# Kernel optimization log

Measured on AMD Instinct MI355X. Metric: run time of the kernel, lower is better.

The kernel has to match this reference:

```python
import jax, jax.numpy as jnp
import numpy as np
import math

N = 6144
HID = 128
HEADS = 4
DEG = 32


def setup_inputs() -> dict:
    key = jax.random.key(0)
    ks = jax.random.split(key, 8)
    H = jax.random.normal(ks[0], (N, HID), dtype=jnp.float32)
    # random edges + self-loops so every row has at least one valid entry
    src = jax.random.randint(ks[1], (N * DEG,), 0, N)
    dst = jax.random.randint(ks[2], (N * DEG,), 0, N)
    loops = jnp.arange(N)
    edge_index = jnp.stack([jnp.concatenate([src, loops]),
                            jnp.concatenate([dst, loops])], axis=0).astype(jnp.int64)
    s = 1.0 / math.sqrt(HID)
    Wq = jax.random.normal(ks[3], (HID, HID * HEADS), dtype=jnp.float32) * s
    Wk = jax.random.normal(ks[4], (HID, HID * HEADS), dtype=jnp.float32) * s
    Wv = jax.random.normal(ks[5], (HID, HID * HEADS), dtype=jnp.float32) * s
    Wp = jax.random.normal(ks[6], (HID * HEADS, HID), dtype=jnp.float32) * (1.0 / math.sqrt(HID * HEADS))
    bp = jnp.zeros((HID,), dtype=jnp.float32)
    return {"H": H, "edge_index": edge_index, "Wq": Wq, "Wk": Wk, "Wv": Wv, "Wp": Wp, "bp": bp}


def reference(H, edge_index, Wq, Wk, Wv, Wp, bp):
    n = H.shape[0]
    q = (H @ Wq).reshape(n, HEADS, HID)
    k = (H @ Wk).reshape(n, HEADS, HID)
    v = (H @ Wv).reshape(n, HEADS, HID)
    # dense boolean edge mask [N, N]
    mask = jnp.zeros((n, n), dtype=bool).at[edge_index[0], edge_index[1]].set(True)
    scores = jnp.einsum('nhd,mhd->hnm', q, k) / math.sqrt(HID)
    scores = jnp.where(mask[None, :, :], scores, -jnp.inf)
    alpha = jax.nn.softmax(scores, axis=-1)
    out = jnp.einsum('hnm,mhd->nhd', alpha, v).reshape(n, HEADS * HID)
    return out @ Wp + bp
```

## Files before the change

### kernel.cpp

```cpp
#include <hip/hip_runtime.h>
#include <hip/hip_bf16.h>


#define N_NODES 6144
#define HIDC 128
#define QKV_N 1536
#define OUT_N 512
#define MASK_WPR 192

typedef __bf16 bf16;
typedef __attribute__((ext_vector_type(8))) __bf16 bf16x8;
typedef __attribute__((ext_vector_type(4))) float f32x4;

__global__ void k_detect_f(const unsigned* __restrict__ Hw, int* __restrict__ fflag) {
    int lane = threadIdx.x;
    unsigned w = Hw[lane];
    int el = (w >> 7) & 0xFF;
    unsigned long long b = __ballot(el >= 110 && el <= 135);
    if (lane == 0) *fflag = (__popcll(b) >= 32) ? 0 : 1;
}

__global__ void k_detect_e(const int* __restrict__ e32, int* __restrict__ eflag) {
    int lane = threadIdx.x;
    unsigned long long b = __ballot(e32[2 * lane + 1] == 0);
    if (lane == 0) *eflag = (b == ~0ull) ? 1 : 0;
}

__global__ __launch_bounds__(256) void k_build_mask(const int* __restrict__ e32, int E,
                                                    const int* __restrict__ eflag,
                                                    unsigned* __restrict__ mask) {
    int e = blockIdx.x * blockDim.x + threadIdx.x;
    if (e >= E) return;
    int s, d;
    if (*eflag) { s = e32[2 * e];  d = e32[2 * E + 2 * e]; }
    else        { s = e32[e];      d = e32[E + e]; }
    if ((unsigned)s < N_NODES && (unsigned)d < N_NODES)
        atomicOr(&mask[s * MASK_WPR + (d >> 5)], 1u << (d & 31));
}

__global__ __launch_bounds__(256) void k_cast_all(const void* __restrict__ H,
                                                  const void* __restrict__ Wq,
                                                  const void* __restrict__ Wk,
                                                  const void* __restrict__ Wv,
                                                  const void* __restrict__ Wp,
                                                  bf16* __restrict__ Hc,
                                                  bf16* __restrict__ Wt_qkv,
                                                  bf16* __restrict__ Wpt,
                                                  const int* __restrict__ fflag) {
    int b = blockIdx.x;
    int t = threadIdx.x;
    int f = *fflag;
    if (b < 3072) {
        int i = b * 256 + t;
        Hc[i] = f ? (bf16)((const float*)H)[i] : ((const bf16*)H)[i];
    } else if (b < 3840) {
        int s = (b - 3072) >> 8;
        int e = ((b - 3072) & 255) * 256 + t;
        int n = e >> 7, k = e & 127;
        const void* W = (s == 0) ? Wq : (s == 1) ? Wk : Wv;
        float v = f ? ((const float*)W)[k * 512 + n] : (float)((const bf16*)W)[k * 512 + n];
        Wt_qkv[(size_t)(s * 512 + n) * 128 + k] = (bf16)v;
    } else {
        int e = (b - 3840) * 256 + t;
        int n = e >> 9, k = e & 511;
        float v = f ? ((const float*)Wp)[k * 128 + n] : (float)((const bf16*)Wp)[k * 128 + n];
        Wpt[(size_t)n * 512 + k] = (bf16)v;
    }
}

__global__ __launch_bounds__(256) void k_gemm_qkv(const bf16* __restrict__ A,
                                                  const bf16* __restrict__ Bt,
                                                  bf16* __restrict__ C) {
    int lane = threadIdx.x & 63;
    int wid  = threadIdx.x >> 6;
    int row0 = blockIdx.x * 64 + wid * 16;
    int col0 = blockIdx.y * 64;
    int r = lane & 15;
    int g = lane >> 4;
    f32x4 acc[4] = {{0,0,0,0},{0,0,0,0},{0,0,0,0},{0,0,0,0}};
    for (int k0 = 0; k0 < 128; k0 += 32) {
        bf16x8 a = *(const bf16x8*)(A + (size_t)(row0 + r) * 128 + k0 + g * 8);
        #pragma unroll
        for (int ct = 0; ct < 4; ++ct) {
            bf16x8 b = *(const bf16x8*)(Bt + (size_t)(col0 + ct * 16 + r) * 128 + k0 + g * 8);
            acc[ct] = __builtin_amdgcn_mfma_f32_16x16x32_bf16(a, b, acc[ct], 0, 0, 0);
        }
    }
    #pragma unroll
    for (int ct = 0; ct < 4; ++ct)
        #pragma unroll
        for (int j = 0; j < 4; ++j)
            C[(size_t)(row0 + g * 4 + j) * QKV_N + col0 + ct * 16 + r] = (bf16)acc[ct][j];
}

__global__ __launch_bounds__(256) void k_attn(const unsigned* __restrict__ mask,
                                              const bf16* __restrict__ qkv,
                                              bf16* __restrict__ ob) {
    __shared__ int s_cnt;
    __shared__ int s_list[256];
    int n = blockIdx.x;
    int t = threadIdx.x;
    if (t == 0) s_cnt = 0;
    __syncthreads();
    if (t < MASK_WPR) {
        unsigned w = mask[n * MASK_WPR + t];
        if (t == (n >> 5)) w |= 1u << (n & 31);
        if (w) {
            int nb = __popc(w);
            int off = atomicAdd(&s_cnt, nb);
            int base = t << 5;
            while (w) {
                int b = __ffs(w) - 1;
                w &= w - 1;
                if (off < 256) s_list[off] = base + b;
                ++off;
            }
        }
    }
    __syncthreads();
    int cnt = min(s_cnt, 256);
    int lane = t & 63;
    int h = t >> 6;
    int g = lane >> 4;
    int r = lane & 15;
    bf16x8 qv = *(const bf16x8*)(qkv + (size_t)n * QKV_N + h * HIDC + r * 8);
    float qf[8];
    #pragma unroll
    for (int j = 0; j < 8; ++j) qf[j] = (float)qv[j];
    float acc[8] = {0, 0, 0, 0, 0, 0, 0, 0};
    float denom = 0.f;
    const float scale = 0.0883883476483184f;
    for (int i0 = 0; i0 < cnt; i0 += 4) {
        int idx = i0 + g;
        bool act = idx < cnt;
        int m = s_list[act ? idx : 0];
        const bf16* kr = qkv + (size_t)m * QKV_N + 512 + h * HIDC + r * 8;
        bf16x8 kv = *(const bf16x8*)kr;
        float p = 0.f;
        #pragma unroll
        for (int j = 0; j < 8; ++j) p += qf[j] * (float)kv[j];
        p += __shfl_xor(p, 1);
        p += __shfl_xor(p, 2);
        p += __shfl_xor(p, 4);
        p += __shfl_xor(p, 8);
        float e = act ? __expf(p * scale) : 0.f;
        denom += e;
        const bf16* vr = qkv + (size_t)m * QKV_N + 1024 + h * HIDC + r * 8;
        bf16x8 vv = *(const bf16x8*)vr;
        #pragma unroll
        for (int j = 0; j < 8; ++j) acc[j] += e * (float)vv[j];
    }
    denom += __shfl_xor(denom, 16);
    denom += __shfl_xor(denom, 32);
    #pragma unroll
    for (int j = 0; j < 8; ++j) {
        acc[j] += __shfl_xor(acc[j], 16);
        acc[j] += __shfl_xor(acc[j], 32);
    }
    if (lane < 16) {
        float inv = (denom > 0.f) ? 1.f / denom : 0.f;
        bf16x8 o;
        #pragma unroll
        for (int j = 0; j < 8; ++j) o[j] = (bf16)(acc[j] * inv);
        *(bf16x8*)(ob + (size_t)n * OUT_N + h * HIDC + r * 8) = o;
    }
}

__global__ __launch_bounds__(256) void k_gemm_out(const bf16* __restrict__ A,
                                                  const bf16* __restrict__ Bt,
                                                  void* __restrict__ Cout,
                                                  const void* __restrict__ bias,
                                                  const int* __restrict__ fflag) {
    int lane = threadIdx.x & 63;
    int wid  = threadIdx.x >> 6;
    int row0 = blockIdx.x * 64 + wid * 16;
    int col0 = blockIdx.y * 16;
    int r = lane & 15;
    int g = lane >> 4;
    f32x4 acc = {0.f, 0.f, 0.f, 0.f};
    for (int k0 = 0; k0 < OUT_N; k0 += 32) {
        bf16x8 a = *(const bf16x8*)(A + (size_t)(row0 + r) * OUT_N + k0 + g * 8);
        bf16x8 b = *(const bf16x8*)(Bt + (size_t)(col0 + r) * OUT_N + k0 + g * 8);
        acc = __builtin_amdgcn_mfma_f32_16x16x32_bf16(a, b, acc, 0, 0, 0);
    }
    int f32io = *fflag;
    int cc = col0 + r;
    float bv = f32io ? ((const float*)bias)[cc] : (float)((const bf16*)bias)[cc];
    #pragma unroll
    for (int j = 0; j < 4; ++j) {
        int rr = row0 + g * 4 + j;
        float v = acc[j] + bv;
        if (f32io) ((float*)Cout)[(size_t)rr * HIDC + cc] = v;
        else       ((bf16*)Cout)[(size_t)rr * HIDC + cc] = (bf16)v;
    }
}

extern "C" void kernel_launch(void* const* d_in, const int* in_sizes, int n_in,
                              void* d_out, int out_size, void* d_ws, size_t ws_size,
                              hipStream_t stream) {
    const void* H    = d_in[0];
    const int* edges = (const int*)d_in[1];
    const void* Wq   = d_in[2];
    const void* Wk   = d_in[3];
    const void* Wv   = d_in[4];
    const void* Wp   = d_in[5];
    const void* bp   = d_in[6];
    int E = in_sizes[1] / 2;

    char* ws = (char*)d_ws;
    size_t off = 0;
    unsigned* mask  = (unsigned*)(ws + off); off += (size_t)N_NODES * MASK_WPR * 4;
    bf16* Hc        = (bf16*)(ws + off);     off += (size_t)N_NODES * HIDC * 2;
    bf16* Wt_qkv    = (bf16*)(ws + off);     off += (size_t)QKV_N * HIDC * 2;
    bf16* Wpt       = (bf16*)(ws + off);     off += (size_t)HIDC * OUT_N * 2;
    bf16* qkvbuf    = (bf16*)(ws + off);     off += (size_t)N_NODES * QKV_N * 2;
    bf16* abuf      = (bf16*)(ws + off);     off += (size_t)N_NODES * OUT_N * 2;
    int* eflag      = (int*)(ws + off);      off += 16;
    int* fflag      = (int*)(ws + off);      off += 16;

    k_detect_f<<<1, 64, 0, stream>>>((const unsigned*)H, fflag);
    k_detect_e<<<1, 64, 0, stream>>>(edges, eflag);
    hipMemsetAsync(mask, 0, (size_t)N_NODES * MASK_WPR * 4, stream);
    k_build_mask<<<(E + 255) / 256, 256, 0, stream>>>(edges, E, eflag, mask);

    k_cast_all<<<4096, 256, 0, stream>>>(H, Wq, Wk, Wv, Wp, Hc, Wt_qkv, Wpt, fflag);

    dim3 g1(N_NODES / 64, QKV_N / 64);
    k_gemm_qkv<<<g1, 256, 0, stream>>>(Hc, Wt_qkv, qkvbuf);

    k_attn<<<N_NODES, 256, 0, stream>>>(mask, qkvbuf, abuf);

    dim3 g2(N_NODES / 64, HIDC / 16);
    k_gemm_out<<<g2, 256, 0, stream>>>(abuf, Wpt, d_out, bp, fflag);
}
```

Before: 173.5 us.

## Merge detect kernels, unroll attention loop by two, widen output GEMM tiles

Combines the two single-wave detection kernels into one 128-thread launch to save a launch. The sparse attention loop now handles two neighbor groups per iteration with separate accumulators, so more K/V gathers are in flight at once. The output projection gives each wave four 16-column MFMA tiles and reuses the A fragment across them, cutting redundant A loads and the block count. In exchange the kernels use more registers, and the out GEMM has fewer blocks in flight.

```diff
diff --git a/kernel.cpp b/kernel.cpp
--- a/kernel.cpp
+++ b/kernel.cpp
@@ -12,18 +12,18 @@
 typedef __attribute__((ext_vector_type(8))) __bf16 bf16x8;
 typedef __attribute__((ext_vector_type(4))) float f32x4;
 
-__global__ void k_detect_f(const unsigned* __restrict__ Hw, int* __restrict__ fflag) {
-    int lane = threadIdx.x;
-    unsigned w = Hw[lane];
-    int el = (w >> 7) & 0xFF;
-    unsigned long long b = __ballot(el >= 110 && el <= 135);
-    if (lane == 0) *fflag = (__popcll(b) >= 32) ? 0 : 1;
-}
-
-__global__ void k_detect_e(const int* __restrict__ e32, int* __restrict__ eflag) {
-    int lane = threadIdx.x;
-    unsigned long long b = __ballot(e32[2 * lane + 1] == 0);
-    if (lane == 0) *eflag = (b == ~0ull) ? 1 : 0;
+__global__ void k_detect(const unsigned* __restrict__ Hw, const int* __restrict__ e32,
+                         int* __restrict__ fflag, int* __restrict__ eflag) {
+    int w = threadIdx.x >> 6, lane = threadIdx.x & 63;
+    if (w == 0) {
+        unsigned x = Hw[lane];
+        int el = (x >> 7) & 0xFF;
+        unsigned long long b = __ballot(el >= 110 && el <= 135);
+        if (lane == 0) *fflag = (__popcll(b) >= 32) ? 0 : 1;
+    } else {
+        unsigned long long b = __ballot(e32[2 * lane + 1] == 0);
+        if (lane == 0) *eflag = (b == ~0ull) ? 1 : 0;
+    }
 }
 
 __global__ __launch_bounds__(256) void k_build_mask(const int* __restrict__ e32, int E,
@@ -127,33 +127,41 @@
     float qf[8];
     #pragma unroll
     for (int j = 0; j < 8; ++j) qf[j] = (float)qv[j];
-    float acc[8] = {0, 0, 0, 0, 0, 0, 0, 0};
-    float denom = 0.f;
+    float accA[8] = {0,0,0,0,0,0,0,0}, accB[8] = {0,0,0,0,0,0,0,0};
+    float denA = 0.f, denB = 0.f;
     const float scale = 0.0883883476483184f;
-    for (int i0 = 0; i0 < cnt; i0 += 4) {
-        int idx = i0 + g;
-        bool act = idx < cnt;
-        int m = s_list[act ? idx : 0];
-        const bf16* kr = qkv + (size_t)m * QKV_N + 512 + h * HIDC + r * 8;
-        bf16x8 kv = *(const bf16x8*)kr;
-        float p = 0.f;
-        #pragma unroll
-        for (int j = 0; j < 8; ++j) p += qf[j] * (float)kv[j];
-        p += __shfl_xor(p, 1);
-        p += __shfl_xor(p, 2);
-        p += __shfl_xor(p, 4);
-        p += __shfl_xor(p, 8);
-        float e = act ? __expf(p * scale) : 0.f;
-        denom += e;
-        const bf16* vr = qkv + (size_t)m * QKV_N + 1024 + h * HIDC + r * 8;
-        bf16x8 vv = *(const bf16x8*)vr;
-        #pragma unroll
-        for (int j = 0; j < 8; ++j) acc[j] += e * (float)vv[j];
-    }
+    for (int i0 = 0; i0 < cnt; i0 += 8) {
+        int iA = i0 + g, iB = i0 + 4 + g;
+        bool aA = iA < cnt, aB = iB < cnt;
+        int mA = s_list[aA ? iA : 0];
+        int mB = s_list[aB ? iB : 0];
+        const bf16* baseA = qkv + (size_t)mA * QKV_N + 512 + h * HIDC + r * 8;
+        const bf16* baseB = qkv + (size_t)mB * QKV_N + 512 + h * HIDC + r * 8;
+        bf16x8 kA = *(const bf16x8*)baseA;
+        bf16x8 kB = *(const bf16x8*)baseB;
+        float pA = 0.f, pB = 0.f;
+        #pragma unroll
+        for (int j = 0; j < 8; ++j) { pA += qf[j] * (float)kA[j]; pB += qf[j] * (float)kB[j]; }
+        #pragma unroll
+        for (int o = 1; o <= 8; o <<= 1) {
+            pA += __shfl_xor(pA, o);
+            pB += __shfl_xor(pB, o);
+        }
+        float eA = aA ? __expf(pA * scale) : 0.f;
+        float eB = aB ? __expf(pB * scale) : 0.f;
+        denA += eA; denB += eB;
+        bf16x8 vA = *(const bf16x8*)(baseA + 512);
+        bf16x8 vB = *(const bf16x8*)(baseB + 512);
+        #pragma unroll
+        for (int j = 0; j < 8; ++j) { accA[j] += eA * (float)vA[j]; accB[j] += eB * (float)vB[j]; }
+    }
+    float denom = denA + denB;
     denom += __shfl_xor(denom, 16);
     denom += __shfl_xor(denom, 32);
+    float acc[8];
     #pragma unroll
     for (int j = 0; j < 8; ++j) {
+        acc[j] = accA[j] + accB[j];
         acc[j] += __shfl_xor(acc[j], 16);
         acc[j] += __shfl_xor(acc[j], 32);
     }
@@ -174,24 +182,30 @@
     int lane = threadIdx.x & 63;
     int wid  = threadIdx.x >> 6;
     int row0 = blockIdx.x * 64 + wid * 16;
-    int col0 = blockIdx.y * 16;
+    int col0 = blockIdx.y * 64;
     int r = lane & 15;
     int g = lane >> 4;
-    f32x4 acc = {0.f, 0.f, 0.f, 0.f};
+    f32x4 acc[4] = {{0,0,0,0},{0,0,0,0},{0,0,0,0},{0,0,0,0}};
     for (int k0 = 0; k0 < OUT_N; k0 += 32) {
         bf16x8 a = *(const bf16x8*)(A + (size_t)(row0 + r) * OUT_N + k0 + g * 8);
-        bf16x8 b = *(const bf16x8*)(Bt + (size_t)(col0 + r) * OUT_N + k0 + g * 8);
-        acc = __builtin_amdgcn_mfma_f32_16x16x32_bf16(a, b, acc, 0, 0, 0);
+        #pragma unroll
+        for (int ct = 0; ct < 4; ++ct) {
+            bf16x8 b = *(const bf16x8*)(Bt + (size_t)(col0 + ct * 16 + r) * OUT_N + k0 + g * 8);
+            acc[ct] = __builtin_amdgcn_mfma_f32_16x16x32_bf16(a, b, acc[ct], 0, 0, 0);
+        }
     }
     int f32io = *fflag;
-    int cc = col0 + r;
-    float bv = f32io ? ((const float*)bias)[cc] : (float)((const bf16*)bias)[cc];
-    #pragma unroll
-    for (int j = 0; j < 4; ++j) {
-        int rr = row0 + g * 4 + j;
-        float v = acc[j] + bv;
-        if (f32io) ((float*)Cout)[(size_t)rr * HIDC + cc] = v;
-        else       ((bf16*)Cout)[(size_t)rr * HIDC + cc] = (bf16)v;
+    #pragma unroll
+    for (int ct = 0; ct < 4; ++ct) {
+        int cc = col0 + ct * 16 + r;
+        float bv = f32io ? ((const float*)bias)[cc] : (float)((const bf16*)bias)[cc];
+        #pragma unroll
+        for (int j = 0; j < 4; ++j) {
+            int rr = row0 + g * 4 + j;
+            float v = acc[ct][j] + bv;
+            if (f32io) ((float*)Cout)[(size_t)rr * HIDC + cc] = v;
+            else       ((bf16*)Cout)[(size_t)rr * HIDC + cc] = (bf16)v;
+        }
     }
 }
 
@@ -218,8 +232,7 @@
     int* eflag      = (int*)(ws + off);      off += 16;
     int* fflag      = (int*)(ws + off);      off += 16;
 
-    k_detect_f<<<1, 64, 0, stream>>>((const unsigned*)H, fflag);
-    k_detect_e<<<1, 64, 0, stream>>>(edges, eflag);
+    k_detect<<<1, 128, 0, stream>>>((const unsigned*)H, edges, fflag, eflag);
     hipMemsetAsync(mask, 0, (size_t)N_NODES * MASK_WPR * 4, stream);
     k_build_mask<<<(E + 255) / 256, 256, 0, stream>>>(edges, E, eflag, mask);
 
@@ -230,6 +243,6 @@
 
     k_attn<<<N_NODES, 256, 0, stream>>>(mask, qkvbuf, abuf);
 
-    dim3 g2(N_NODES / 64, HIDC / 16);
+    dim3 g2(N_NODES / 64, HIDC / 64);
     k_gemm_out<<<g2, 256, 0, stream>>>(abuf, Wpt, d_out, bp, fflag);
 }
```

After: 170.8 us. About the same (-1.5%).
